# Kernel tuning notes

Hardware: AMD Instinct MI355X
Metric: run time of the kernel (lower is better)

Reference implementation:

```python
import jax, jax.numpy as jnp
import numpy as np

DIM = 1024
HEADS = 16
HEAD_DIM = DIM // HEADS


def setup_inputs() -> dict:
    key = jax.random.key(0)
    k1, k2, k3, k4 = jax.random.split(key, 4)
    x = jax.random.normal(k1, (4, 4096, DIM), dtype=jnp.float32)
    # nn.Linear(dim, 3*dim, bias=False): weight [3*dim, dim]
    w_qkv = jax.random.normal(k2, (3 * DIM, DIM), dtype=jnp.float32) * (DIM ** -0.5)
    # nn.Linear(dim, dim): weight [dim, dim], bias [dim]
    w_proj = jax.random.normal(k3, (DIM, DIM), dtype=jnp.float32) * (DIM ** -0.5)
    b_proj = jax.random.normal(k4, (DIM,), dtype=jnp.float32) * 0.01
    return {"x": x, "w_qkv": w_qkv, "w_proj": w_proj, "b_proj": b_proj}


def reference(x, w_qkv, w_proj, b_proj):
    B, N, C = x.shape
    H, D = HEADS, HEAD_DIM
    qkv = x @ w_qkv.T                                    # [B, N, 3C]
    qkv = qkv.reshape(B, N, 3, H, D).transpose(2, 0, 3, 1, 4)  # [3, B, H, N, D]
    q, k, v = qkv[0], qkv[1], qkv[2]
    # elu(x) + 1 feature map (positive kernel)
    q = jax.nn.elu(q) + 1.0
    k = jax.nn.elu(k) + 1.0
    kv = jnp.einsum('bhnd,bhne->bhde', k, v)             # [B, H, D, D]
    num = jnp.einsum('bhnd,bhde->bhne', q, kv)           # [B, H, N, D]
    k_sum = k.sum(axis=-2)                               # [B, H, D]
    qk = jnp.einsum('bhnd,bhd->bhn', q, k_sum)[..., None]  # [B, H, N, 1]
    out = num / (qk + 1e-8)                              # [B, H, N, D]
    out = out.transpose(0, 2, 1, 3).reshape(B, N, C)
    return out @ w_proj.T + b_proj
```

## Files before the change

kernel.cpp:

```cpp
#include <hip/hip_runtime.h>
#include <hip/hip_bf16.h>
#include <stdint.h>

typedef __hip_bfloat16 bf16;
typedef __attribute__((ext_vector_type(4))) float f32x4;
typedef __attribute__((ext_vector_type(8))) short short8;

#define SEQ   4096
#define CDIM  1024

__device__ __forceinline__ void async_load16(const void* g, void* l) {
  auto gp = reinterpret_cast<const __attribute__((address_space(1))) uint32_t*>(
      reinterpret_cast<uintptr_t>(g));
  auto lp = reinterpret_cast<__attribute__((address_space(3))) uint32_t*>(
      static_cast<uint32_t>(reinterpret_cast<uintptr_t>(l)));
  __builtin_amdgcn_global_load_lds(gp, lp, 16, 0, 0);
}

__global__ __launch_bounds__(256) void convert3_kernel(const float* __restrict__ x,
                                                       const float* __restrict__ wq,
                                                       const float* __restrict__ wp,
                                                       bf16* __restrict__ xb,
                                                       bf16* __restrict__ wqb,
                                                       bf16* __restrict__ wpb) {
  int i = blockIdx.x * 256 + threadIdx.x;
  const float* src;
  bf16* dst;
  int off;
  if (i < 4194304)      { src = x;  dst = xb;  off = i; }
  else if (i < 4980736) { src = wq; dst = wqb; off = i - 4194304; }
  else                  { src = wp; dst = wpb; off = i - 4980736; }
  float4 f = ((const float4*)src)[off];
  union { bf16 b[4]; ushort4 u; } c;
  c.b[0] = __float2bfloat16(f.x);
  c.b[1] = __float2bfloat16(f.y);
  c.b[2] = __float2bfloat16(f.z);
  c.b[3] = __float2bfloat16(f.w);
  ((ushort4*)dst)[off] = c.u;
}

#define BARR()  __builtin_amdgcn_s_barrier()
#define LGKM0() asm volatile("s_waitcnt lgkmcnt(0)" ::: "memory")
#define VMW6()  asm volatile("s_waitcnt vmcnt(6)" ::: "memory")
#define VMW0()  asm volatile("s_waitcnt vmcnt(0)" ::: "memory")
#define SP(x)   __builtin_amdgcn_s_setprio(x)

#define STA(buf, kc, h)                                                        \
  {                                                                            \
    const int ra_ = (h) * 64 + w * 8;                                          \
    async_load16(Ag + (size_t)(ra_ + lr8) * K + (kc) + cs, (buf) + ra_ * 64);  \
    async_load16(Ag + (size_t)(ra_ + 128 + lr8) * K + (kc) + cs,               \
                 (buf) + (ra_ + 128) * 64);                                    \
  }
#define STB(buf, kc, h)                                                        \
  {                                                                            \
    const int rb_ = (w & 3) * 8 + (w >> 2) * 64 + (h) * 32;                    \
    async_load16(Bg + (size_t)(rb_ + lr8) * K + (kc) + cs, (buf) + rb_ * 64);  \
    async_load16(Bg + (size_t)(rb_ + 128 + lr8) * K + (kc) + cs,               \
                 (buf) + (rb_ + 128) * 64);                                    \
  }

#define RD_A(buf, h)                                                           \
  {                                                                            \
    _Pragma("unroll") for (int mi = 0; mi < 4; ++mi) {                         \
      const unsigned short* p_ = (buf) + (arow0 + (h) * 64 + mi * 16) * 64;    \
      af[mi][0] = *(const short8*)(p_ + ((lq * 8) ^ sw));                      \
      af[mi][1] = *(const short8*)(p_ + ((32 + lq * 8) ^ sw));                 \
    }                                                                          \
  }
#define RD_B(buf, h)                                                           \
  {                                                                            \
    _Pragma("unroll") for (int ni = 0; ni < 2; ++ni) {                         \
      const unsigned short* p_ = (buf) + (brow0 + (h) * 32 + ni * 16) * 64;    \
      bfr[h][ni][0] = *(const short8*)(p_ + ((lq * 8) ^ sw));                  \
      bfr[h][ni][1] = *(const short8*)(p_ + ((32 + lq * 8) ^ sw));             \
    }                                                                          \
  }

#define MMA(MQ, NQ)                                                            \
  {                                                                            \
    _Pragma("unroll") for (int ks = 0; ks < 2; ++ks)                           \
      _Pragma("unroll") for (int mi = 0; mi < 4; ++mi)                         \
        _Pragma("unroll") for (int ni = 0; ni < 2; ++ni)                       \
          acc[(MQ) * 4 + mi][(NQ) * 2 + ni] =                                  \
              __builtin_amdgcn_mfma_f32_16x16x32_bf16(                         \
                  af[mi][ks], bfr[NQ][ni][ks],                                 \
                  acc[(MQ) * 4 + mi][(NQ) * 2 + ni], 0, 0, 0);                 \
  }

#define FULL_ITER(kc)                                                          \
  RD_A(A0, 0); RD_B(B0, 0); STB(B1, (kc) + 64, 0);                             \
  BARR(); LGKM0(); SP(1); MMA(0, 0); SP(0); BARR();                            \
  RD_B(B0, 1); STA(A0, (kc) + 128, 0);                                         \
  BARR(); LGKM0(); SP(1); MMA(0, 1); SP(0); BARR();                            \
  RD_A(A0, 1); STB(B0, (kc) + 128, 1);                                         \
  BARR(); LGKM0(); SP(1); MMA(1, 1); SP(0); BARR();                            \
  STA(A0, (kc) + 128, 1); VMW6();                                              \
  BARR(); SP(1); MMA(1, 0); SP(0); BARR();                                     \
  RD_A(A1, 0); RD_B(B1, 0); STB(B0, (kc) + 128, 0);                            \
  BARR(); LGKM0(); SP(1); MMA(0, 0); SP(0); BARR();                            \
  RD_B(B1, 1); STA(A1, (kc) + 192, 0);                                         \
  BARR(); LGKM0(); SP(1); MMA(0, 1); SP(0); BARR();                            \
  RD_A(A1, 1); STB(B1, (kc) + 192, 1);                                         \
  BARR(); LGKM0(); SP(1); MMA(1, 1); SP(0); BARR();                            \
  STA(A1, (kc) + 192, 1); VMW6();                                              \
  BARR(); SP(1); MMA(1, 0); SP(0); BARR();

#define FINAL_ITER(kc)                                                         \
  RD_A(A0, 0); RD_B(B0, 0); STB(B1, (kc) + 64, 0);                             \
  BARR(); LGKM0(); SP(1); MMA(0, 0); SP(0); BARR();                            \
  RD_B(B0, 1);                                                                 \
  BARR(); LGKM0(); SP(1); MMA(0, 1); SP(0); BARR();                            \
  RD_A(A0, 1);                                                                 \
  BARR(); LGKM0(); SP(1); MMA(1, 1); SP(0); BARR();                            \
  VMW0();                                                                      \
  BARR(); SP(1); MMA(1, 0); SP(0); BARR();                                     \
  RD_A(A1, 0); RD_B(B1, 0);                                                    \
  BARR(); LGKM0(); SP(1); MMA(0, 0); SP(0); BARR();                            \
  RD_B(B1, 1);                                                                 \
  BARR(); LGKM0(); SP(1); MMA(0, 1); SP(0); BARR();                            \
  RD_A(A1, 1);                                                                 \
  BARR(); LGKM0(); SP(1); MMA(1, 1); SP(0); BARR();                            \
  SP(1); MMA(1, 0); SP(0);

template <int EPI>
__global__ __launch_bounds__(512, 2) void gemm256(const bf16* __restrict__ X,
                                                  const bf16* __restrict__ W,
                                                  const float* __restrict__ bias,
                                                  bf16* __restrict__ Qo,
                                                  bf16* __restrict__ Ko,
                                                  bf16* __restrict__ Vo,
                                                  float* __restrict__ Out,
                                                  const int K) {
  __shared__ __attribute__((aligned(16))) unsigned short lds[4][256 * 64];
  unsigned short* const A0 = lds[0];
  unsigned short* const B0 = lds[1];
  unsigned short* const A1 = lds[2];
  unsigned short* const B1 = lds[3];

  const int tid  = threadIdx.x;
  const int w    = tid >> 6, lane = tid & 63;
  const int wm   = w >> 2,   wn   = w & 3;
  const int lr   = lane & 15, lq  = lane >> 4;

  const int GX   = (int)gridDim.x;
  const int nwg  = GX * (int)gridDim.y;
  const int lin  = (int)blockIdx.y * GX + (int)blockIdx.x;
  const int tile = (lin & 7) * (nwg >> 3) + (lin >> 3);
  const int bn   = tile % GX;
  const int bm   = tile / GX;

  const int sw   = (lr & 7) << 3;
  const int cs   = (((lane & 7) ^ (lane >> 3)) << 3);
  const int lr8  = lane >> 3;

  const bool swapped = (EPI == 0) && (bn < 4);
  const bf16* Xg = X + (size_t)(bm * 256) * K;
  const bf16* Wg = W + (size_t)(bn * 256) * K;
  const bf16* Ag = swapped ? Wg : Xg;
  const bf16* Bg = swapped ? Xg : Wg;

  const int arow0 = wm * 128 + lr;
  const int brow0 = wn * 64 + lr;

  short8 af[4][2], bfr[2][2][2];
  f32x4 acc[8][4] = {};

  STA(A0, 0, 0);
  STB(B0, 0, 0);
  STB(B0, 0, 1);
  STA(A0, 0, 1);
  STA(A1, 64, 0);
  STB(B1, 64, 1);
  STA(A1, 64, 1);
  VMW6();
  BARR();

#pragma unroll 1
  for (int kc = 0; kc < K - 128; kc += 128) {
    FULL_ITER(kc);
  }
  FINAL_ITER(K - 128);

  if constexpr (EPI == 0) {
    if (swapped) {
#pragma unroll
      for (int mt = 0; mt < 8; ++mt) {
        const int j0 = bn * 256 + wm * 128 + mt * 16 + lq * 4;
        const int h  = j0 >> 6, d0 = j0 & 63;
#pragma unroll
        for (int nt = 0; nt < 4; ++nt) {
          const int t = bm * 256 + wn * 64 + nt * 16 + lr;
          const int b = t >> 12, n = t & 4095;
          union { bf16 v[4]; ushort4 u; } pk;
#pragma unroll
          for (int r = 0; r < 4; ++r) {
            float v = acc[mt][nt][r];
            v = (v > 0.0f) ? (v + 1.0f) : __expf(v);
            pk.v[r] = __float2bfloat16(v);
          }
          *(ushort4*)(Qo + (((size_t)((b * 16 + h) * SEQ + n)) << 6) + d0) = pk.u;
        }
      }
    } else {
#pragma unroll
      for (int nt = 0; nt < 4; ++nt) {
        const int j   = bn * 256 + wn * 64 + nt * 16 + lr;
        const int sel = j >> 10;
        const int h   = (j >> 6) & 15;
        const int d   = j & 63;
        bf16* dst = (sel == 1) ? Ko : Vo;
#pragma unroll
        for (int mt = 0; mt < 8; ++mt) {
          const int t0 = bm * 256 + wm * 128 + mt * 16 + lq * 4;
          const int b = t0 >> 12, n0 = t0 & 4095;
          union { bf16 v[4]; ushort4 u; } pk;
#pragma unroll
          for (int r = 0; r < 4; ++r) {
            float v = acc[mt][nt][r];
            if (sel == 1) v = (v > 0.0f) ? (v + 1.0f) : __expf(v);
            pk.v[r] = __float2bfloat16(v);
          }
          *(ushort4*)(dst + ((size_t)((b * 16 + h) * 64 + d)) * SEQ + n0) = pk.u;
        }
      }
    }
  } else {
#pragma unroll
    for (int mt = 0; mt < 8; ++mt) {
#pragma unroll
      for (int r = 0; r < 4; ++r) {
        const int t = bm * 256 + wm * 128 + mt * 16 + lq * 4 + r;
        float* op = Out + (size_t)t * CDIM + bn * 256 + wn * 64 + lr;
#pragma unroll
        for (int nt = 0; nt < 4; ++nt)
          op[nt * 16] = acc[mt][nt][r] + bias[bn * 256 + wn * 64 + nt * 16 + lr];
      }
    }
  }
}

__global__ __launch_bounds__(256) void kv_mfma(const bf16* __restrict__ KT,
                                               const bf16* __restrict__ VT,
                                               float* __restrict__ KVp,
                                               float* __restrict__ KSp) {
  __shared__ bf16 kt[64 * 64];
  __shared__ bf16 vt[64 * 64];
  const int tid = threadIdx.x;
  const int w = tid >> 6, lane = tid & 63;
  const int wm = w >> 1, wn = w & 1;
  const int lr = lane & 15, lq = lane >> 4;
  const int swz = (lr & 7) * 8;
  const int csz = (((lane & 7) ^ (lane >> 3)) * 8);
  const int sp = blockIdx.x, bh = blockIdx.y;
  const bf16* kg0 = KT + (size_t)bh * 64 * SEQ + sp * 512;
  const bf16* vg0 = VT + (size_t)bh * 64 * SEQ + sp * 512;

  f32x4 acc[2][2] = {};
  f32x4 kacc0 = {}, kacc1 = {};
  short8 ones;
#pragma unroll
  for (int j = 0; j < 8; ++j) ((unsigned short*)&ones)[j] = 0x3F80;

  for (int nc = 0; nc < 8; ++nc) {
    __syncthreads();
#pragma unroll
    for (int i = 0; i < 2; ++i) {
      const int row = w * 16 + i * 8 + (lane >> 3);
      async_load16(kg0 + (size_t)row * SEQ + nc * 64 + csz, kt + (w * 16 + i * 8) * 64);
      async_load16(vg0 + (size_t)row * SEQ + nc * 64 + csz, vt + (w * 16 + i * 8) * 64);
    }
    __syncthreads();

#pragma unroll
    for (int ks = 0; ks < 2; ++ks) {
      short8 a0 = *(const short8*)&kt[(wm * 32 +      lr) * 64 + ((ks * 32 + lq * 8) ^ swz)];
      short8 a1 = *(const short8*)&kt[(wm * 32 + 16 + lr) * 64 + ((ks * 32 + lq * 8) ^ swz)];
      short8 b0 = *(const short8*)&vt[(wn * 32 +      lr) * 64 + ((ks * 32 + lq * 8) ^ swz)];
      short8 b1 = *(const short8*)&vt[(wn * 32 + 16 + lr) * 64 + ((ks * 32 + lq * 8) ^ swz)];
      acc[0][0] = __builtin_amdgcn_mfma_f32_16x16x32_bf16(a0, b0, acc[0][0], 0, 0, 0);
      acc[0][1] = __builtin_amdgcn_mfma_f32_16x16x32_bf16(a0, b1, acc[0][1], 0, 0, 0);
      acc[1][0] = __builtin_amdgcn_mfma_f32_16x16x32_bf16(a1, b0, acc[1][0], 0, 0, 0);
      acc[1][1] = __builtin_amdgcn_mfma_f32_16x16x32_bf16(a1, b1, acc[1][1], 0, 0, 0);
      kacc0 = __builtin_amdgcn_mfma_f32_16x16x32_bf16(a0, ones, kacc0, 0, 0, 0);
      kacc1 = __builtin_amdgcn_mfma_f32_16x16x32_bf16(a1, ones, kacc1, 0, 0, 0);
    }
  }

  float* outp = KVp + ((size_t)(sp * 64 + bh)) * 4096;
#pragma unroll
  for (int mt = 0; mt < 2; ++mt)
#pragma unroll
    for (int nt = 0; nt < 2; ++nt) {
      const int e  = wn * 32 + nt * 16 + lr;
      const int d0 = wm * 32 + mt * 16 + lq * 4;
      *(float4*)&outp[e * 64 + d0] = *(float4*)&acc[mt][nt];
    }
  if (wn == 0 && lr == 0) {
    float* ksp = KSp + (size_t)(sp * 64 + bh) * 64 + wm * 32;
#pragma unroll
    for (int r = 0; r < 4; ++r) {
      ksp[lq * 4 + r]      = kacc0[r];
      ksp[16 + lq * 4 + r] = kacc1[r];
    }
  }
}

__global__ __launch_bounds__(256) void kv_reduce(const float* __restrict__ KVp,
                                                 const float* __restrict__ KSp,
                                                 bf16* __restrict__ KVT,
                                                 float* __restrict__ KS) {
  const int bh = blockIdx.x >> 2, q = blockIdx.x & 3, t = threadIdx.x;
#pragma unroll
  for (int i = 0; i < 4; ++i) {
    const int idx = (q * 4 + i) * 256 + t;
    float s = 0.0f;
#pragma unroll
    for (int sp = 0; sp < 8; ++sp) s += KVp[((size_t)(sp * 64 + bh)) * 4096 + idx];
    const bf16 hi = __float2bfloat16(s);
    const float lo = s - __bfloat162float(hi);
    const int e = idx >> 6, d = idx & 63;
    KVT[(size_t)bh * 8192 + e * 128 + d]      = hi;
    KVT[(size_t)bh * 8192 + e * 128 + 64 + d] = __float2bfloat16(lo);
  }
  if (q == 0 && t < 64) {
    float s = 0.0f;
#pragma unroll
    for (int sp = 0; sp < 8; ++sp) s += KSp[(sp * 64 + bh) * 64 + t];
    KS[bh * 64 + t] = s;
  }
}

__global__ __launch_bounds__(256) void num_mfma(const bf16* __restrict__ Qb,
                                                const bf16* __restrict__ KVT,
                                                const float* __restrict__ KS,
                                                bf16* __restrict__ Attn) {
  __shared__ bf16 qs[128 * 64];
  __shared__ bf16 kvs[64 * 128];
  __shared__ bf16 Cs[128 * 72];
  __shared__ float ksl[64];
  __shared__ float dred[256];
  __shared__ float den[128];
  const int tid = threadIdx.x;
  const int w = tid >> 6, lane = tid & 63;
  const int wm = w >> 1, wn = w & 1;
  const int lr = lane & 15, lq = lane >> 4;
  const int swz = (lr & 7) * 8;
  const int bh = blockIdx.y, n00 = blockIdx.x * 128;
  const int b = bh >> 4, h = bh & 15;

  const bf16* qg  = Qb  + ((size_t)bh * SEQ + n00) * 64;
  const bf16* kvg = KVT + (size_t)bh * 8192;
  const int qcs = (((lane & 7) ^ (lane >> 3)) * 8);
#pragma unroll
  for (int i = 0; i < 4; ++i) {
    const int row = w * 32 + i * 8 + (lane >> 3);
    async_load16(qg + (size_t)row * 64 + qcs, qs + (w * 32 + i * 8) * 64);
  }
#pragma unroll
  for (int i = 0; i < 4; ++i) {
    const int row = w * 16 + i * 4 + (lane >> 4);
    const int scol = (((lane & 15) * 8) ^ ((row & 7) * 8));
    async_load16(kvg + (size_t)row * 128 + scol, kvs + (w * 16 + i * 4) * 128);
  }
  if (tid < 64) ksl[tid] = KS[bh * 64 + tid];
  __syncthreads();

  {
    const int n = tid >> 1, half = tid & 1;
    const int nsw = (n & 7) * 8;
    float s = 0.0f;
#pragma unroll
    for (int v8 = 0; v8 < 4; ++v8) {
      short8 qq = *(const short8*)&qs[n * 64 + ((half * 32 + v8 * 8) ^ nsw)];
#pragma unroll
      for (int j = 0; j < 8; ++j)
        s += __bfloat162float(((const bf16*)&qq)[j]) * ksl[half * 32 + v8 * 8 + j];
    }
    dred[tid] = s;
  }

  short8 afr[4][2], bfr2[2][4];
#pragma unroll
  for (int mt = 0; mt < 4; ++mt)
#pragma unroll
    for (int kh = 0; kh < 2; ++kh)
      afr[mt][kh] = *(const short8*)&qs[(wm * 64 + mt * 16 + lr) * 64 + ((kh * 32 + lq * 8) ^ swz)];
#pragma unroll
  for (int nt = 0; nt < 2; ++nt)
#pragma unroll
    for (int ks = 0; ks < 4; ++ks)
      bfr2[nt][ks] = *(const short8*)&kvs[(wn * 32 + nt * 16 + lr) * 128 + ((ks * 32 + lq * 8) ^ swz)];

  f32x4 acc[4][2] = {};
#pragma unroll
  for (int ks = 0; ks < 4; ++ks)
#pragma unroll
    for (int mt = 0; mt < 4; ++mt)
#pragma unroll
      for (int nt = 0; nt < 2; ++nt)
        acc[mt][nt] = __builtin_amdgcn_mfma_f32_16x16x32_bf16(afr[mt][ks & 1], bfr2[nt][ks],
                                                              acc[mt][nt], 0, 0, 0);
  __syncthreads();
  if (tid < 128) den[tid] = dred[tid * 2] + dred[tid * 2 + 1] + 1e-8f;
  __syncthreads();

#pragma unroll
  for (int mt = 0; mt < 4; ++mt) {
#pragma unroll
    for (int r = 0; r < 4; ++r) {
      const int nl = wm * 64 + mt * 16 + lq * 4 + r;
      const float inv = 1.0f / den[nl];
#pragma unroll
      for (int nt = 0; nt < 2; ++nt) {
        const int e = wn * 32 + nt * 16 + lr;
        Cs[nl * 72 + e] = __float2bfloat16(acc[mt][nt][r] * inv);
      }
    }
  }
  __syncthreads();
#pragma unroll
  for (int it = 0; it < 4; ++it) {
    const int nl = it * 32 + (tid >> 3);
    const int ch = tid & 7;
    short8 val = *(const short8*)&Cs[nl * 72 + ch * 8];
    *(short8*)(Attn + ((size_t)(b * SEQ + n00 + nl)) * CDIM + h * 64 + ch * 8) = val;
  }
}

extern "C" void kernel_launch(void* const* d_in, const int* in_sizes, int n_in,
                              void* d_out, int out_size, void* d_ws, size_t ws_size,
                              hipStream_t stream) {
  const float* x      = (const float*)d_in[0];
  const float* w_qkv  = (const float*)d_in[1];
  const float* w_proj = (const float*)d_in[2];
  const float* b_proj = (const float*)d_in[3];
  float* out = (float*)d_out;
  char* ws = (char*)d_ws;

  bf16*  xb     = (bf16*)(ws + 0);
  bf16*  wqkvb  = (bf16*)(ws + 33554432);
  bf16*  wprojb = (bf16*)(ws + 39845888);
  bf16*  qb     = (bf16*)(ws + 41943040);
  bf16*  ktb    = (bf16*)(ws + 75497472);
  bf16*  vtb    = (bf16*)(ws + 109051904);
  float* kvp    = (float*)(ws + 0);
  float* ksp    = (float*)(ws + 8388608);
  bf16*  kvt    = (bf16*)(ws + 142606336);
  float* ksum   = (float*)(ws + 143654912);
  bf16*  attn   = (bf16*)(ws + 0);

  convert3_kernel<<<20480, 256, 0, stream>>>(x, w_qkv, w_proj, xb, wqkvb, wprojb);

  gemm256<0><<<dim3(12, 64), 512, 0, stream>>>(xb, wqkvb, nullptr, qb, ktb, vtb, nullptr, 1024);
  kv_mfma<<<dim3(8, 64), 256, 0, stream>>>(ktb, vtb, kvp, ksp);
  kv_reduce<<<256, 256, 0, stream>>>(kvp, ksp, kvt, ksum);
  num_mfma<<<dim3(32, 64), 256, 0, stream>>>(qb, kvt, ksum, attn);
  gemm256<1><<<dim3(4, 64), 512, 0, stream>>>(attn, wprojb, b_proj, nullptr, nullptr, nullptr, out, 1024);
}
```

Measured before the change: 304.9 us.

## Make QKV GEMM persistent with cross-tile prefetch and nontemporal loads/stores

The QKV GEMM becomes a persistent kernel of 256 workgroups, each processing three 256x256 tiles in sequence. It prefetches the next tile's first K-chunks during the current tile's last iteration, so the pipeline does not drain between tiles. The per-workgroup XCD-aware tile swizzle is dropped in favour of a simple linear id stride, which may hurt L2 locality. Loads in the convert kernel and all epilogue stores now use nontemporal hints to reduce cache pollution.

Measured after the change: 341.2 us. 1.12x slower.

```diff
diff --git a/kernel.cpp b/kernel.cpp
--- a/kernel.cpp
+++ b/kernel.cpp
@@ -5,6 +5,7 @@
 typedef __hip_bfloat16 bf16;
 typedef __attribute__((ext_vector_type(4))) float f32x4;
 typedef __attribute__((ext_vector_type(8))) short short8;
+typedef __attribute__((ext_vector_type(4))) unsigned short u16x4;
 
 #define SEQ   4096
 #define CDIM  1024
@@ -30,13 +31,13 @@
   if (i < 4194304)      { src = x;  dst = xb;  off = i; }
   else if (i < 4980736) { src = wq; dst = wqb; off = i - 4194304; }
   else                  { src = wp; dst = wpb; off = i - 4980736; }
-  float4 f = ((const float4*)src)[off];
-  union { bf16 b[4]; ushort4 u; } c;
-  c.b[0] = __float2bfloat16(f.x);
-  c.b[1] = __float2bfloat16(f.y);
-  c.b[2] = __float2bfloat16(f.z);
-  c.b[3] = __float2bfloat16(f.w);
-  ((ushort4*)dst)[off] = c.u;
+  f32x4 f = __builtin_nontemporal_load(((const f32x4*)src) + off);
+  union { bf16 b[4]; u16x4 u; } c;
+  c.b[0] = __float2bfloat16(f[0]);
+  c.b[1] = __float2bfloat16(f[1]);
+  c.b[2] = __float2bfloat16(f[2]);
+  c.b[3] = __float2bfloat16(f[3]);
+  ((u16x4*)dst)[off] = c.u;
 }
 
 #define BARR()  __builtin_amdgcn_s_barrier()
@@ -45,18 +46,20 @@
 #define VMW0()  asm volatile("s_waitcnt vmcnt(0)" ::: "memory")
 #define SP(x)   __builtin_amdgcn_s_setprio(x)
 
-#define STA(buf, kc, h)                                                        \
+#define STA(buf, base, kc, h)                                                  \
   {                                                                            \
     const int ra_ = (h) * 64 + w * 8;                                          \
-    async_load16(Ag + (size_t)(ra_ + lr8) * K + (kc) + cs, (buf) + ra_ * 64);  \
-    async_load16(Ag + (size_t)(ra_ + 128 + lr8) * K + (kc) + cs,               \
+    async_load16((base) + (size_t)(ra_ + lr8) * K + (kc) + cs,                 \
+                 (buf) + ra_ * 64);                                            \
+    async_load16((base) + (size_t)(ra_ + 128 + lr8) * K + (kc) + cs,           \
                  (buf) + (ra_ + 128) * 64);                                    \
   }
-#define STB(buf, kc, h)                                                        \
+#define STB(buf, base, kc, h)                                                  \
   {                                                                            \
     const int rb_ = (w & 3) * 8 + (w >> 2) * 64 + (h) * 32;                    \
-    async_load16(Bg + (size_t)(rb_ + lr8) * K + (kc) + cs, (buf) + rb_ * 64);  \
-    async_load16(Bg + (size_t)(rb_ + 128 + lr8) * K + (kc) + cs,               \
+    async_load16((base) + (size_t)(rb_ + lr8) * K + (kc) + cs,                 \
+                 (buf) + rb_ * 64);                                            \
+    async_load16((base) + (size_t)(rb_ + 128 + lr8) * K + (kc) + cs,           \
                  (buf) + (rb_ + 128) * 64);                                    \
   }
 
@@ -88,26 +91,26 @@
                   acc[(MQ) * 4 + mi][(NQ) * 2 + ni], 0, 0, 0);                 \
   }
 
-#define FULL_ITER(kc)                                                          \
-  RD_A(A0, 0); RD_B(B0, 0); STB(B1, (kc) + 64, 0);                             \
+#define FULL_ITER_BODY()                                                       \
+  RD_A(A0, 0); RD_B(B0, 0); STB(B1, BgC, kl + 64, 0);                          \
   BARR(); LGKM0(); SP(1); MMA(0, 0); SP(0); BARR();                            \
-  RD_B(B0, 1); STA(A0, (kc) + 128, 0);                                         \
+  RD_B(B0, 1); STA(A0, sA, k1, 0);                                             \
   BARR(); LGKM0(); SP(1); MMA(0, 1); SP(0); BARR();                            \
-  RD_A(A0, 1); STB(B0, (kc) + 128, 1);                                         \
+  RD_A(A0, 1); STB(B0, sB, k1, 1);                                             \
   BARR(); LGKM0(); SP(1); MMA(1, 1); SP(0); BARR();                            \
-  STA(A0, (kc) + 128, 1); VMW6();                                              \
+  STA(A0, sA, k1, 1); VMW6();                                                  \
   BARR(); SP(1); MMA(1, 0); SP(0); BARR();                                     \
-  RD_A(A1, 0); RD_B(B1, 0); STB(B0, (kc) + 128, 0);                            \
+  RD_A(A1, 0); RD_B(B1, 0); STB(B0, sB, k1, 0);                                \
   BARR(); LGKM0(); SP(1); MMA(0, 0); SP(0); BARR();                            \
-  RD_B(B1, 1); STA(A1, (kc) + 192, 0);                                         \
+  RD_B(B1, 1); STA(A1, sA, k2, 0);                                             \
   BARR(); LGKM0(); SP(1); MMA(0, 1); SP(0); BARR();                            \
-  RD_A(A1, 1); STB(B1, (kc) + 192, 1);                                         \
+  RD_A(A1, 1); STB(B1, sB, k2, 1);                                             \
   BARR(); LGKM0(); SP(1); MMA(1, 1); SP(0); BARR();                            \
-  STA(A1, (kc) + 192, 1); VMW6();                                              \
+  STA(A1, sA, k2, 1); VMW6();                                                  \
   BARR(); SP(1); MMA(1, 0); SP(0); BARR();
 
-#define FINAL_ITER(kc)                                                         \
-  RD_A(A0, 0); RD_B(B0, 0); STB(B1, (kc) + 64, 0);                             \
+#define FINAL_ITER_BODY()                                                      \
+  RD_A(A0, 0); RD_B(B0, 0); STB(B1, BgC, 960, 0);                              \
   BARR(); LGKM0(); SP(1); MMA(0, 0); SP(0); BARR();                            \
   RD_B(B0, 1);                                                                 \
   BARR(); LGKM0(); SP(1); MMA(0, 1); SP(0); BARR();                            \
@@ -123,7 +126,7 @@
   BARR(); LGKM0(); SP(1); MMA(1, 1); SP(0); BARR();                            \
   SP(1); MMA(1, 0); SP(0);
 
-template <int EPI>
+template <int EPI, int NTILES, int GNX>
 __global__ __launch_bounds__(512, 2) void gemm256(const bf16* __restrict__ X,
                                                   const bf16* __restrict__ W,
                                                   const float* __restrict__ bias,
@@ -143,101 +146,139 @@
   const int wm   = w >> 2,   wn   = w & 3;
   const int lr   = lane & 15, lq  = lane >> 4;
 
-  const int GX   = (int)gridDim.x;
-  const int nwg  = GX * (int)gridDim.y;
-  const int lin  = (int)blockIdx.y * GX + (int)blockIdx.x;
-  const int tile = (lin & 7) * (nwg >> 3) + (lin >> 3);
-  const int bn   = tile % GX;
-  const int bm   = tile / GX;
-
   const int sw   = (lr & 7) << 3;
   const int cs   = (((lane & 7) ^ (lane >> 3)) << 3);
   const int lr8  = lane >> 3;
 
-  const bool swapped = (EPI == 0) && (bn < 4);
-  const bf16* Xg = X + (size_t)(bm * 256) * K;
-  const bf16* Wg = W + (size_t)(bn * 256) * K;
-  const bf16* Ag = swapped ? Wg : Xg;
-  const bf16* Bg = swapped ? Xg : Wg;
-
   const int arow0 = wm * 128 + lr;
   const int brow0 = wn * 64 + lr;
 
+  int id = (int)blockIdx.x;
+  int bn = id % GNX, bm = id / GNX;
+  bool swapped = (EPI == 0) && (bn < 4);
+  const bf16* AgC;
+  const bf16* BgC;
+  const bf16* AgX;
+  const bf16* BgX;
+  {
+    const bf16* Xg = X + (size_t)(bm * 256) * K;
+    const bf16* Wg = W + (size_t)(bn * 256) * K;
+    AgC = swapped ? Wg : Xg;
+    BgC = swapped ? Xg : Wg;
+    const int idX = id + 256;
+    const int bnX = idX % GNX, bmX = idX / GNX;
+    const bool swX = (EPI == 0) && (bnX < 4);
+    const bf16* XgX = X + (size_t)(bmX * 256) * K;
+    const bf16* WgX = W + (size_t)(bnX * 256) * K;
+    AgX = swX ? WgX : XgX;
+    BgX = swX ? XgX : WgX;
+  }
+
   short8 af[4][2], bfr[2][2][2];
   f32x4 acc[8][4] = {};
 
-  STA(A0, 0, 0);
-  STB(B0, 0, 0);
-  STB(B0, 0, 1);
-  STA(A0, 0, 1);
-  STA(A1, 64, 0);
-  STB(B1, 64, 1);
-  STA(A1, 64, 1);
-  VMW6();
-  BARR();
-
-#pragma unroll 1
-  for (int kc = 0; kc < K - 128; kc += 128) {
-    FULL_ITER(kc);
-  }
-  FINAL_ITER(K - 128);
-
-  if constexpr (EPI == 0) {
-    if (swapped) {
-#pragma unroll
-      for (int mt = 0; mt < 8; ++mt) {
-        const int j0 = bn * 256 + wm * 128 + mt * 16 + lq * 4;
-        const int h  = j0 >> 6, d0 = j0 & 63;
+  auto epilogue = [&](int bmv, int bnv, bool swv) {
+    if constexpr (EPI == 0) {
+      if (swv) {
+#pragma unroll
+        for (int mt = 0; mt < 8; ++mt) {
+          const int j0 = bnv * 256 + wm * 128 + mt * 16 + lq * 4;
+          const int hh = j0 >> 6, d0 = j0 & 63;
+#pragma unroll
+          for (int nt = 0; nt < 4; ++nt) {
+            const int t = bmv * 256 + wn * 64 + nt * 16 + lr;
+            const int b = t >> 12, n = t & 4095;
+            union { bf16 v[4]; u16x4 u; } pk;
+#pragma unroll
+            for (int r = 0; r < 4; ++r) {
+              float v = acc[mt][nt][r];
+              v = (v > 0.0f) ? (v + 1.0f) : __expf(v);
+              pk.v[r] = __float2bfloat16(v);
+            }
+            __builtin_nontemporal_store(
+                pk.u, (u16x4*)(Qo + (((size_t)((b * 16 + hh) * SEQ + n)) << 6) + d0));
+          }
+        }
+      } else {
 #pragma unroll
         for (int nt = 0; nt < 4; ++nt) {
-          const int t = bm * 256 + wn * 64 + nt * 16 + lr;
-          const int b = t >> 12, n = t & 4095;
-          union { bf16 v[4]; ushort4 u; } pk;
-#pragma unroll
-          for (int r = 0; r < 4; ++r) {
-            float v = acc[mt][nt][r];
-            v = (v > 0.0f) ? (v + 1.0f) : __expf(v);
-            pk.v[r] = __float2bfloat16(v);
+          const int ch  = bnv * 256 + wn * 64 + nt * 16 + lr;
+          const int sel = ch >> 10;
+          const int hh  = (ch >> 6) & 15;
+          const int d   = ch & 63;
+          bf16* dst = (sel == 1) ? Ko : Vo;
+#pragma unroll
+          for (int mt = 0; mt < 8; ++mt) {
+            const int t0 = bmv * 256 + wm * 128 + mt * 16 + lq * 4;
+            const int b = t0 >> 12, n0 = t0 & 4095;
+            union { bf16 v[4]; u16x4 u; } pk;
+#pragma unroll
+            for (int r = 0; r < 4; ++r) {
+              float v = acc[mt][nt][r];
+              if (sel == 1) v = (v > 0.0f) ? (v + 1.0f) : __expf(v);
+              pk.v[r] = __float2bfloat16(v);
+            }
+            __builtin_nontemporal_store(
+                pk.u, (u16x4*)(dst + ((size_t)((b * 16 + hh) * 64 + d)) * SEQ + n0));
           }
-          *(ushort4*)(Qo + (((size_t)((b * 16 + h) * SEQ + n)) << 6) + d0) = pk.u;
         }
       }
     } else {
 #pragma unroll
-      for (int nt = 0; nt < 4; ++nt) {
-        const int j   = bn * 256 + wn * 64 + nt * 16 + lr;
-        const int sel = j >> 10;
-        const int h   = (j >> 6) & 15;
-        const int d   = j & 63;
-        bf16* dst = (sel == 1) ? Ko : Vo;
-#pragma unroll
-        for (int mt = 0; mt < 8; ++mt) {
-          const int t0 = bm * 256 + wm * 128 + mt * 16 + lq * 4;
-          const int b = t0 >> 12, n0 = t0 & 4095;
-          union { bf16 v[4]; ushort4 u; } pk;
-#pragma unroll
-          for (int r = 0; r < 4; ++r) {
-            float v = acc[mt][nt][r];
-            if (sel == 1) v = (v > 0.0f) ? (v + 1.0f) : __expf(v);
-            pk.v[r] = __float2bfloat16(v);
-          }
-          *(ushort4*)(dst + ((size_t)((b * 16 + h) * 64 + d)) * SEQ + n0) = pk.u;
+      for (int mt = 0; mt < 8; ++mt) {
+#pragma unroll
+        for (int r = 0; r < 4; ++r) {
+          const int t = bmv * 256 + wm * 128 + mt * 16 + lq * 4 + r;
+          float* op = Out + (size_t)t * CDIM + bnv * 256 + wn * 64 + lr;
+#pragma unroll
+          for (int nt = 0; nt < 4; ++nt)
+            __builtin_nontemporal_store(
+                acc[mt][nt][r] + bias[bnv * 256 + wn * 64 + nt * 16 + lr],
+                op + nt * 16);
         }
       }
     }
-  } else {
-#pragma unroll
-    for (int mt = 0; mt < 8; ++mt) {
-#pragma unroll
-      for (int r = 0; r < 4; ++r) {
-        const int t = bm * 256 + wm * 128 + mt * 16 + lq * 4 + r;
-        float* op = Out + (size_t)t * CDIM + bn * 256 + wn * 64 + lr;
-#pragma unroll
-        for (int nt = 0; nt < 4; ++nt)
-          op[nt * 16] = acc[mt][nt][r] + bias[bn * 256 + wn * 64 + nt * 16 + lr];
-      }
-    }
-  }
+  };
+
+  STA(A0, AgC, 0, 0);
+  STB(B0, BgC, 0, 0);
+  STB(B0, BgC, 0, 1);
+  STA(A0, AgC, 0, 1);
+  STA(A1, AgC, 64, 0);
+  STB(B1, BgC, 64, 1);
+  STA(A1, AgC, 64, 1);
+  VMW6();
+  BARR();
+
+#pragma unroll 1
+  for (int j = 0; j < 8 * NTILES - 1; ++j) {
+    const int kl = (j & 7) << 7;
+    const bf16* sA = AgC;
+    const bf16* sB = BgC;
+    int k1 = kl + 128, k2 = kl + 192;
+    if (k1 == 1024) { sA = AgX; sB = BgX; k1 = 0; k2 = 64; }
+    FULL_ITER_BODY();
+    if ((j & 7) == 7) {
+      epilogue(bm, bn, swapped);
+#pragma unroll
+      for (int mi = 0; mi < 8; ++mi)
+#pragma unroll
+        for (int ni = 0; ni < 4; ++ni) acc[mi][ni] = (f32x4){0.f, 0.f, 0.f, 0.f};
+      id += 256;
+      bn = id % GNX; bm = id / GNX;
+      swapped = (EPI == 0) && (bn < 4);
+      AgC = AgX; BgC = BgX;
+      const int idX = id + 256;
+      const int bnX = idX % GNX, bmX = idX / GNX;
+      const bool swX = (EPI == 0) && (bnX < 4);
+      const bf16* XgX = X + (size_t)(bmX * 256) * K;
+      const bf16* WgX = W + (size_t)(bnX * 256) * K;
+      AgX = swX ? WgX : XgX;
+      BgX = swX ? XgX : WgX;
+    }
+  }
+  FINAL_ITER_BODY();
+  epilogue(bm, bn, swapped);
 }
 
 __global__ __launch_bounds__(256) void kv_mfma(const bf16* __restrict__ KT,
@@ -452,9 +493,9 @@
 
   convert3_kernel<<<20480, 256, 0, stream>>>(x, w_qkv, w_proj, xb, wqkvb, wprojb);
 
-  gemm256<0><<<dim3(12, 64), 512, 0, stream>>>(xb, wqkvb, nullptr, qb, ktb, vtb, nullptr, 1024);
+  gemm256<0, 3, 12><<<256, 512, 0, stream>>>(xb, wqkvb, nullptr, qb, ktb, vtb, nullptr, 1024);
   kv_mfma<<<dim3(8, 64), 256, 0, stream>>>(ktb, vtb, kvp, ksp);
   kv_reduce<<<256, 256, 0, stream>>>(kvp, ksp, kvt, ksum);
   num_mfma<<<dim3(32, 64), 256, 0, stream>>>(qb, kvt, ksum, attn);
-  gemm256<1><<<dim3(4, 64), 512, 0, stream>>>(attn, wprojb, b_proj, nullptr, nullptr, nullptr, out, 1024);
-}
+  gemm256<1, 1, 4><<<256, 512, 0, stream>>>(attn, wprojb, b_proj, nullptr, nullptr, nullptr, out, 1024);
+}
```

## Software-pipeline LDS fragment reads across MFMA phases in GEMM main loop

Applied to the files above, without the earlier changes.

Restructures the 8-phase GEMM loop so LDS reads of the next A half and B0 fragments are issued right after the current MFMA block, overlapping them with later work. Partial lgkmcnt(4) waits and sched_barrier replace the full waits and the double barrier around each phase. B0 fragments are double-buffered in registers, which raises register pressure. FINAL_ITER now hardcodes a K offset of 960, so it assumes K=1024.

After: 329.7 us. +8.1%, slower.

```diff
diff --git a/kernel.cpp b/kernel.cpp
--- a/kernel.cpp
+++ b/kernel.cpp
@@ -39,11 +39,13 @@
   ((ushort4*)dst)[off] = c.u;
 }
 
-#define BARR()  __builtin_amdgcn_s_barrier()
-#define LGKM0() asm volatile("s_waitcnt lgkmcnt(0)" ::: "memory")
-#define VMW6()  asm volatile("s_waitcnt vmcnt(6)" ::: "memory")
-#define VMW0()  asm volatile("s_waitcnt vmcnt(0)" ::: "memory")
-#define SP(x)   __builtin_amdgcn_s_setprio(x)
+#define BARR()   __builtin_amdgcn_s_barrier()
+#define LGKM0_() asm volatile("s_waitcnt lgkmcnt(0)" ::: "memory")
+#define LGKM4_() asm volatile("s_waitcnt lgkmcnt(4)" ::: "memory")
+#define VMW6()   asm volatile("s_waitcnt vmcnt(6)" ::: "memory")
+#define VMW0()   asm volatile("s_waitcnt vmcnt(0)" ::: "memory")
+#define SP(x)    __builtin_amdgcn_s_setprio(x)
+#define SB0()    __builtin_amdgcn_sched_barrier(0)
 
 #define STA(buf, kc, h)                                                        \
   {                                                                            \
@@ -60,7 +62,7 @@
                  (buf) + (rb_ + 128) * 64);                                    \
   }
 
-#define RD_A(buf, h)                                                           \
+#define RD_AH(buf, h)                                                          \
   {                                                                            \
     _Pragma("unroll") for (int mi = 0; mi < 4; ++mi) {                         \
       const unsigned short* p_ = (buf) + (arow0 + (h) * 64 + mi * 16) * 64;    \
@@ -68,60 +70,70 @@
       af[mi][1] = *(const short8*)(p_ + ((32 + lq * 8) ^ sw));                 \
     }                                                                          \
   }
-#define RD_B(buf, h)                                                           \
+#define RD_B1(buf)                                                             \
   {                                                                            \
     _Pragma("unroll") for (int ni = 0; ni < 2; ++ni) {                         \
-      const unsigned short* p_ = (buf) + (brow0 + (h) * 32 + ni * 16) * 64;    \
-      bfr[h][ni][0] = *(const short8*)(p_ + ((lq * 8) ^ sw));                  \
-      bfr[h][ni][1] = *(const short8*)(p_ + ((32 + lq * 8) ^ sw));             \
+      const unsigned short* p_ = (buf) + (brow0 + 32 + ni * 16) * 64;          \
+      b1r[ni][0] = *(const short8*)(p_ + ((lq * 8) ^ sw));                     \
+      b1r[ni][1] = *(const short8*)(p_ + ((32 + lq * 8) ^ sw));                \
     }                                                                          \
   }
-
-#define MMA(MQ, NQ)                                                            \
+#define RD_B0S(buf, S)                                                         \
+  {                                                                            \
+    _Pragma("unroll") for (int ni = 0; ni < 2; ++ni) {                         \
+      const unsigned short* p_ = (buf) + (brow0 + ni * 16) * 64;               \
+      b0r[S][ni][0] = *(const short8*)(p_ + ((lq * 8) ^ sw));                  \
+      b0r[S][ni][1] = *(const short8*)(p_ + ((32 + lq * 8) ^ sw));             \
+    }                                                                          \
+  }
+
+#define MMA_B0(MQ, S)                                                          \
   {                                                                            \
     _Pragma("unroll") for (int ks = 0; ks < 2; ++ks)                           \
       _Pragma("unroll") for (int mi = 0; mi < 4; ++mi)                         \
         _Pragma("unroll") for (int ni = 0; ni < 2; ++ni)                       \
-          acc[(MQ) * 4 + mi][(NQ) * 2 + ni] =                                  \
-              __builtin_amdgcn_mfma_f32_16x16x32_bf16(                         \
-                  af[mi][ks], bfr[NQ][ni][ks],                                 \
-                  acc[(MQ) * 4 + mi][(NQ) * 2 + ni], 0, 0, 0);                 \
+          acc[(MQ) * 4 + mi][ni] = __builtin_amdgcn_mfma_f32_16x16x32_bf16(    \
+              af[mi][ks], b0r[S][ni][ks], acc[(MQ) * 4 + mi][ni], 0, 0, 0);    \
+  }
+#define MMA_B1(MQ)                                                             \
+  {                                                                            \
+    _Pragma("unroll") for (int ks = 0; ks < 2; ++ks)                           \
+      _Pragma("unroll") for (int mi = 0; mi < 4; ++mi)                         \
+        _Pragma("unroll") for (int ni = 0; ni < 2; ++ni)                       \
+          acc[(MQ) * 4 + mi][2 + ni] = __builtin_amdgcn_mfma_f32_16x16x32_bf16(\
+              af[mi][ks], b1r[ni][ks], acc[(MQ) * 4 + mi][2 + ni], 0, 0, 0);   \
   }
 
 #define FULL_ITER(kc)                                                          \
-  RD_A(A0, 0); RD_B(B0, 0); STB(B1, (kc) + 64, 0);                             \
-  BARR(); LGKM0(); SP(1); MMA(0, 0); SP(0); BARR();                            \
-  RD_B(B0, 1); STA(A0, (kc) + 128, 0);                                         \
-  BARR(); LGKM0(); SP(1); MMA(0, 1); SP(0); BARR();                            \
-  RD_A(A0, 1); STB(B0, (kc) + 128, 1);                                         \
-  BARR(); LGKM0(); SP(1); MMA(1, 1); SP(0); BARR();                            \
-  STA(A0, (kc) + 128, 1); VMW6();                                              \
-  BARR(); SP(1); MMA(1, 0); SP(0); BARR();                                     \
-  RD_A(A1, 0); RD_B(B1, 0); STB(B0, (kc) + 128, 0);                            \
-  BARR(); LGKM0(); SP(1); MMA(0, 0); SP(0); BARR();                            \
-  RD_B(B1, 1); STA(A1, (kc) + 192, 0);                                         \
-  BARR(); LGKM0(); SP(1); MMA(0, 1); SP(0); BARR();                            \
-  RD_A(A1, 1); STB(B1, (kc) + 192, 1);                                         \
-  BARR(); LGKM0(); SP(1); MMA(1, 1); SP(0); BARR();                            \
-  STA(A1, (kc) + 192, 1); VMW6();                                              \
-  BARR(); SP(1); MMA(1, 0); SP(0); BARR();
-
-#define FINAL_ITER(kc)                                                         \
-  RD_A(A0, 0); RD_B(B0, 0); STB(B1, (kc) + 64, 0);                             \
-  BARR(); LGKM0(); SP(1); MMA(0, 0); SP(0); BARR();                            \
-  RD_B(B0, 1);                                                                 \
-  BARR(); LGKM0(); SP(1); MMA(0, 1); SP(0); BARR();                            \
-  RD_A(A0, 1);                                                                 \
-  BARR(); LGKM0(); SP(1); MMA(1, 1); SP(0); BARR();                            \
-  VMW0();                                                                      \
-  BARR(); SP(1); MMA(1, 0); SP(0); BARR();                                     \
-  RD_A(A1, 0); RD_B(B1, 0);                                                    \
-  BARR(); LGKM0(); SP(1); MMA(0, 0); SP(0); BARR();                            \
-  RD_B(B1, 1);                                                                 \
-  BARR(); LGKM0(); SP(1); MMA(0, 1); SP(0); BARR();                            \
-  RD_A(A1, 1);                                                                 \
-  BARR(); LGKM0(); SP(1); MMA(1, 1); SP(0); BARR();                            \
-  SP(1); MMA(1, 0); SP(0);
+  BARR(); STB(B1, (kc) + 64, 0); RD_B1(B0);                                    \
+  LGKM4_(); SB0(); SP(1); MMA_B0(0, 0); SP(0);                                 \
+  BARR(); STA(A0, (kc) + 128, 0);                                              \
+  LGKM0_(); SB0(); SP(1); MMA_B1(0); SP(0); RD_AH(A0, 1);                      \
+  BARR(); STB(B0, (kc) + 128, 1);                                              \
+  LGKM0_(); SB0(); SP(1); MMA_B1(1); SP(0);                                    \
+  BARR(); STA(A0, (kc) + 128, 1); VMW6(); BARR(); RD_B0S(B1, 1);               \
+  LGKM4_(); SB0(); SP(1); MMA_B0(1, 0); SP(0); RD_AH(A1, 0);                   \
+  BARR(); STB(B0, (kc) + 128, 0); RD_B1(B1);                                   \
+  LGKM4_(); SB0(); SP(1); MMA_B0(0, 1); SP(0);                                 \
+  BARR(); STA(A1, (kc) + 192, 0);                                              \
+  LGKM0_(); SB0(); SP(1); MMA_B1(0); SP(0); RD_AH(A1, 1);                      \
+  BARR(); STB(B1, (kc) + 192, 1);                                              \
+  LGKM0_(); SB0(); SP(1); MMA_B1(1); SP(0);                                    \
+  BARR(); STA(A1, (kc) + 192, 1); VMW6(); BARR(); RD_B0S(B0, 0);               \
+  LGKM4_(); SB0(); SP(1); MMA_B0(1, 1); SP(0); RD_AH(A0, 0);
+
+#define FINAL_ITER()                                                           \
+  BARR(); STB(B1, 960, 0); RD_B1(B0);                                          \
+  LGKM4_(); SB0(); SP(1); MMA_B0(0, 0); SP(0);                                 \
+  BARR(); LGKM0_(); SB0(); SP(1); MMA_B1(0); SP(0); RD_AH(A0, 1);              \
+  BARR(); LGKM0_(); SB0(); SP(1); MMA_B1(1); SP(0);                            \
+  BARR(); VMW0(); BARR(); RD_B0S(B1, 1);                                       \
+  LGKM4_(); SB0(); SP(1); MMA_B0(1, 0); SP(0); RD_AH(A1, 0);                   \
+  BARR(); RD_B1(B1);                                                           \
+  LGKM4_(); SB0(); SP(1); MMA_B0(0, 1); SP(0);                                 \
+  BARR(); LGKM0_(); SB0(); SP(1); MMA_B1(0); SP(0); RD_AH(A1, 1);              \
+  BARR(); LGKM0_(); SB0(); SP(1); MMA_B1(1); SP(0);                            \
+  BARR(); LGKM0_(); SB0(); SP(1); MMA_B0(1, 1); SP(0);
 
 template <int EPI>
 __global__ __launch_bounds__(512, 2) void gemm256(const bf16* __restrict__ X,
@@ -163,7 +175,9 @@
   const int arow0 = wm * 128 + lr;
   const int brow0 = wn * 64 + lr;
 
-  short8 af[4][2], bfr[2][2][2];
+  short8 af[4][2];
+  short8 b1r[2][2];
+  short8 b0r[2][2][2];
   f32x4 acc[8][4] = {};
 
   STA(A0, 0, 0);
@@ -175,12 +189,14 @@
   STA(A1, 64, 1);
   VMW6();
   BARR();
+  RD_AH(A0, 0);
+  RD_B0S(B0, 0);
 
 #pragma unroll 1
   for (int kc = 0; kc < K - 128; kc += 128) {
     FULL_ITER(kc);
   }
-  FINAL_ITER(K - 128);
+  FINAL_ITER();
 
   if constexpr (EPI == 0) {
     if (swapped) {
```

## Double-buffer kv_mfma loads and split sequence into 16 chunks

Applied to the files above, without the earlier changes.

kv_mfma now stages K/V tiles into two LDS buffers so the async load of the next chunk overlaps MFMA work on the current one. The sequence split per block is halved (256 instead of 512 tokens), doubling the grid to 16x64 blocks for more parallelism. kv_reduce sums 16 partials instead of 8 and the KS partial buffer offset moves to make room. This adds LDS use and more partial-sum traffic in the reduce step.

Result: no change. 309.3 us (+1.4%).

```diff
diff --git a/kernel.cpp b/kernel.cpp
--- a/kernel.cpp
+++ b/kernel.cpp
@@ -42,6 +42,7 @@
 #define BARR()  __builtin_amdgcn_s_barrier()
 #define LGKM0() asm volatile("s_waitcnt lgkmcnt(0)" ::: "memory")
 #define VMW6()  asm volatile("s_waitcnt vmcnt(6)" ::: "memory")
+#define VMW4()  asm volatile("s_waitcnt vmcnt(4)" ::: "memory")
 #define VMW0()  asm volatile("s_waitcnt vmcnt(0)" ::: "memory")
 #define SP(x)   __builtin_amdgcn_s_setprio(x)
 
@@ -244,8 +245,8 @@
                                                const bf16* __restrict__ VT,
                                                float* __restrict__ KVp,
                                                float* __restrict__ KSp) {
-  __shared__ bf16 kt[64 * 64];
-  __shared__ bf16 vt[64 * 64];
+  __shared__ bf16 kt[2][64 * 64];
+  __shared__ bf16 vt[2][64 * 64];
   const int tid = threadIdx.x;
   const int w = tid >> 6, lane = tid & 63;
   const int wm = w >> 1, wn = w & 1;
@@ -253,8 +254,8 @@
   const int swz = (lr & 7) * 8;
   const int csz = (((lane & 7) ^ (lane >> 3)) * 8);
   const int sp = blockIdx.x, bh = blockIdx.y;
-  const bf16* kg0 = KT + (size_t)bh * 64 * SEQ + sp * 512;
-  const bf16* vg0 = VT + (size_t)bh * 64 * SEQ + sp * 512;
+  const bf16* kg0 = KT + (size_t)bh * 64 * SEQ + sp * 256;
+  const bf16* vg0 = VT + (size_t)bh * 64 * SEQ + sp * 256;
 
   f32x4 acc[2][2] = {};
   f32x4 kacc0 = {}, kacc1 = {};
@@ -262,22 +263,31 @@
 #pragma unroll
   for (int j = 0; j < 8; ++j) ((unsigned short*)&ones)[j] = 0x3F80;
 
-  for (int nc = 0; nc < 8; ++nc) {
-    __syncthreads();
-#pragma unroll
-    for (int i = 0; i < 2; ++i) {
-      const int row = w * 16 + i * 8 + (lane >> 3);
-      async_load16(kg0 + (size_t)row * SEQ + nc * 64 + csz, kt + (w * 16 + i * 8) * 64);
-      async_load16(vg0 + (size_t)row * SEQ + nc * 64 + csz, vt + (w * 16 + i * 8) * 64);
-    }
-    __syncthreads();
-
+#define KVSTG(b, c)                                                            \
+  {                                                                            \
+    _Pragma("unroll") for (int i = 0; i < 2; ++i) {                            \
+      const int row = w * 16 + i * 8 + (lane >> 3);                            \
+      async_load16(kg0 + (size_t)row * SEQ + (c) * 64 + csz,                   \
+                   &kt[b][(w * 16 + i * 8) * 64]);                             \
+      async_load16(vg0 + (size_t)row * SEQ + (c) * 64 + csz,                   \
+                   &vt[b][(w * 16 + i * 8) * 64]);                             \
+    }                                                                          \
+  }
+
+  KVSTG(0, 0);
+  KVSTG(1, 1);
+  VMW4();
+  __syncthreads();
+
+#pragma unroll
+  for (int c = 0; c < 4; ++c) {
+    const int b = c & 1;
 #pragma unroll
     for (int ks = 0; ks < 2; ++ks) {
-      short8 a0 = *(const short8*)&kt[(wm * 32 +      lr) * 64 + ((ks * 32 + lq * 8) ^ swz)];
-      short8 a1 = *(const short8*)&kt[(wm * 32 + 16 + lr) * 64 + ((ks * 32 + lq * 8) ^ swz)];
-      short8 b0 = *(const short8*)&vt[(wn * 32 +      lr) * 64 + ((ks * 32 + lq * 8) ^ swz)];
-      short8 b1 = *(const short8*)&vt[(wn * 32 + 16 + lr) * 64 + ((ks * 32 + lq * 8) ^ swz)];
+      short8 a0 = *(const short8*)&kt[b][(wm * 32 +      lr) * 64 + ((ks * 32 + lq * 8) ^ swz)];
+      short8 a1 = *(const short8*)&kt[b][(wm * 32 + 16 + lr) * 64 + ((ks * 32 + lq * 8) ^ swz)];
+      short8 b0 = *(const short8*)&vt[b][(wn * 32 +      lr) * 64 + ((ks * 32 + lq * 8) ^ swz)];
+      short8 b1 = *(const short8*)&vt[b][(wn * 32 + 16 + lr) * 64 + ((ks * 32 + lq * 8) ^ swz)];
       acc[0][0] = __builtin_amdgcn_mfma_f32_16x16x32_bf16(a0, b0, acc[0][0], 0, 0, 0);
       acc[0][1] = __builtin_amdgcn_mfma_f32_16x16x32_bf16(a0, b1, acc[0][1], 0, 0, 0);
       acc[1][0] = __builtin_amdgcn_mfma_f32_16x16x32_bf16(a1, b0, acc[1][0], 0, 0, 0);
@@ -285,7 +295,16 @@
       kacc0 = __builtin_amdgcn_mfma_f32_16x16x32_bf16(a0, ones, kacc0, 0, 0, 0);
       kacc1 = __builtin_amdgcn_mfma_f32_16x16x32_bf16(a1, ones, kacc1, 0, 0, 0);
     }
-  }
+    __syncthreads();
+    if (c < 2) {
+      KVSTG(b, c + 2);
+      VMW4();
+    } else if (c == 2) {
+      VMW0();
+    }
+    __syncthreads();
+  }
+#undef KVSTG
 
   float* outp = KVp + ((size_t)(sp * 64 + bh)) * 4096;
 #pragma unroll
@@ -316,7 +335,7 @@
     const int idx = (q * 4 + i) * 256 + t;
     float s = 0.0f;
 #pragma unroll
-    for (int sp = 0; sp < 8; ++sp) s += KVp[((size_t)(sp * 64 + bh)) * 4096 + idx];
+    for (int sp = 0; sp < 16; ++sp) s += KVp[((size_t)(sp * 64 + bh)) * 4096 + idx];
     const bf16 hi = __float2bfloat16(s);
     const float lo = s - __bfloat162float(hi);
     const int e = idx >> 6, d = idx & 63;
@@ -326,7 +345,7 @@
   if (q == 0 && t < 64) {
     float s = 0.0f;
 #pragma unroll
-    for (int sp = 0; sp < 8; ++sp) s += KSp[(sp * 64 + bh) * 64 + t];
+    for (int sp = 0; sp < 16; ++sp) s += KSp[(sp * 64 + bh) * 64 + t];
     KS[bh * 64 + t] = s;
   }
 }
@@ -445,7 +464,7 @@
   bf16*  ktb    = (bf16*)(ws + 75497472);
   bf16*  vtb    = (bf16*)(ws + 109051904);
   float* kvp    = (float*)(ws + 0);
-  float* ksp    = (float*)(ws + 8388608);
+  float* ksp    = (float*)(ws + 16777216);
   bf16*  kvt    = (bf16*)(ws + 142606336);
   float* ksum   = (float*)(ws + 143654912);
   bf16*  attn   = (bf16*)(ws + 0);
@@ -453,7 +472,7 @@
   convert3_kernel<<<20480, 256, 0, stream>>>(x, w_qkv, w_proj, xb, wqkvb, wprojb);
 
   gemm256<0><<<dim3(12, 64), 512, 0, stream>>>(xb, wqkvb, nullptr, qb, ktb, vtb, nullptr, 1024);
-  kv_mfma<<<dim3(8, 64), 256, 0, stream>>>(ktb, vtb, kvp, ksp);
+  kv_mfma<<<dim3(16, 64), 256, 0, stream>>>(ktb, vtb, kvp, ksp);
   kv_reduce<<<256, 256, 0, stream>>>(kvp, ksp, kvt, ksum);
   num_mfma<<<dim3(32, 64), 256, 0, stream>>>(qb, kvt, ksum, attn);
   gemm256<1><<<dim3(4, 64), 512, 0, stream>>>(attn, wprojb, b_proj, nullptr, nullptr, nullptr, out, 1024);
```
